# Performance work log

Hardware: AMD Instinct MI355X
Metric: run time of the kernel (lower is better)

Reference implementation:

```python
import jax, jax.numpy as jnp
import numpy as np

B, M, D = 8, 1024, 768          # batch, tokens, model dim
N, P = 32, 32                   # experts, slots per expert (N*P == M)
K = 8                           # mix_k (router top-k)
H = 2048                        # expert MLP hidden dim
EPS = 1e-12


def setup_inputs() -> dict:
    key = jax.random.key(0)
    ks = jax.random.split(key, 6)
    std_d = 1.0 / np.sqrt(D)
    std_h = 1.0 / np.sqrt(H)
    return {
        "x": jax.random.normal(ks[0], (B, M, D), jnp.float32),
        "cluster_assignments": jax.random.randint(ks[1], (B, M, K), 0, N),
        "phi": jax.random.normal(ks[2], (D, N, P), jnp.float32) * std_d,
        "scale": jnp.ones((1,), jnp.float32),
        "w1": jax.random.normal(ks[3], (N, D, H), jnp.float32) * std_d,
        "b1": jnp.zeros((N, H), jnp.float32),
        "w2": jax.random.normal(ks[4], (N, H, D), jnp.float32) * std_h,
        "b2": jnp.zeros((N, D), jnp.float32),
    }


def _seg_mean(vals, idx, num_segments):
    # index_reduce(..., 'mean', include_self=False): empty segments stay 0
    s = jax.ops.segment_sum(vals, idx, num_segments=num_segments)
    c = jax.ops.segment_sum(jnp.ones((vals.shape[0], 1), vals.dtype), idx,
                            num_segments=num_segments)
    return jnp.where(c > 0, s / jnp.maximum(c, 1.0), 0.0)


def _compute_acmoe(x_flat, top_assign):
    # MAD-based per-cluster, per-dim scaling (mad=True, mix_weights=False)
    mean_kd = _seg_mean(x_flat, top_assign, N)                 # [N, D]
    centered = jnp.abs(x_flat - mean_kd[top_assign])           # [B*M, D]
    w_mad = _seg_mean(centered, top_assign, N)                 # [N, D]
    W = 1.0 / (w_mad + 0.35)
    top_clamp = 5.0 * W.mean()
    W = jnp.minimum(W, top_clamp)
    W = W / W.mean()
    return W[top_assign]                                       # [B*M, D]


def reference(x, cluster_assignments, phi, scale, w1, b1, w2, b2):
    # normalize tokens (dim=2) and phi (dim=0), scale phi
    xn = x / jnp.maximum(jnp.linalg.norm(x, axis=-1, keepdims=True), EPS)
    phin = scale * phi / jnp.maximum(jnp.linalg.norm(phi, axis=0, keepdims=True), EPS)

    # ACMoE feature re-weighting (no-grad in original)
    top_assign = cluster_assignments.reshape(-1, K)[:, 0]       # [B*M]
    Mw = jax.lax.stop_gradient(_compute_acmoe(
        jax.lax.stop_gradient(xn.reshape(-1, D)), top_assign))
    xn = (xn.reshape(-1, D) * Mw).reshape(B, M, D)

    logits = jnp.einsum('bmd,dnp->bmnp', xn, phin)              # [B,M,N,P]
    aff = logits.reshape(B, M, N * P)
    mixing_weights, slot_assignments = jax.lax.top_k(aff, K)    # [B,M,K]
    new_clusters = slot_assignments // P

    disp = jax.nn.softmax(logits, axis=1)                       # over tokens m
    comb = jax.nn.softmax(aff, axis=-1).reshape(B, M, N, P)     # over (n,p)

    xs = jnp.einsum('bmd,bmnp->bnpd', xn, disp)                 # [B,N,P,D]
    # per-expert MLP, batched over expert axis n
    h = jnp.einsum('bnpd,ndh->bnph', xs, w1) + b1[None, :, None, :]
    h = jax.nn.gelu(h, approximate=False)
    ys = jnp.einsum('bnph,nhd->bnpd', h, w2) + b2[None, :, None, :]

    y = jnp.einsum('bnpd,bmnp->bmd', ys, comb)                  # [B,M,D]
    return y, mixing_weights, new_clusters
```

## Files before the change

### kernel.cpp

```cpp
#include <hip/hip_runtime.h>
#include <cmath>

#define NB    8
#define MTOK  1024
#define BMT   8192
#define DD    768
#define NEXP  32
#define PSLOT 32
#define NP    1024
#define KTOP  8
#define HH    2048

#define SLICES 128
#define TPS    64

typedef unsigned short ushort;
typedef __attribute__((ext_vector_type(8))) short short8v;
typedef __attribute__((ext_vector_type(4))) short short4v;
typedef __attribute__((ext_vector_type(4))) float f32x4;

__device__ __forceinline__ ushort bf16_rne(float x) {
    unsigned u = __float_as_uint(x);
    unsigned r = (u + 0x7FFFu + ((u >> 16) & 1u)) >> 16;
    return (ushort)r;
}
__device__ __forceinline__ float bf16_to_f(ushort h) {
    return __uint_as_float(((unsigned)h) << 16);
}
__device__ __forceinline__ void split2(float x, ushort& hi, ushort& lo) {
    hi = bf16_rne(x);
    lo = bf16_rne(x - bf16_to_f(hi));
}

__device__ __forceinline__ void gl_lds16(const ushort* g, ushort* l) {
    __builtin_amdgcn_global_load_lds(
        (const __attribute__((address_space(1))) void*)g,
        (__attribute__((address_space(3))) void*)l, 16, 0, 0);
}

__global__ __launch_bounds__(256) void norm_x(const float* __restrict__ x, float* __restrict__ xn) {
    int tok = blockIdx.x;
    int t = threadIdx.x;
    const float* p = x + (long)tok * DD;
    float v0 = p[t], v1 = p[t + 256], v2 = p[t + 512];
    float ss = v0 * v0 + v1 * v1 + v2 * v2;
#pragma unroll
    for (int o = 32; o; o >>= 1) ss += __shfl_xor(ss, o);
    __shared__ float sred[4];
    if ((t & 63) == 0) sred[t >> 6] = ss;
    __syncthreads();
    ss = sred[0] + sred[1] + sred[2] + sred[3];
    float inv = 1.0f / fmaxf(sqrtf(ss), 1e-12f);
    float* q = xn + (long)tok * DD;
    q[t] = v0 * inv; q[t + 256] = v1 * inv; q[t + 512] = v2 * inv;
}

__global__ __launch_bounds__(256) void norm_phi_T(const float* __restrict__ phi, const float* __restrict__ scale,
                                                  ushort* __restrict__ phT_hi, ushort* __restrict__ phT_lo) {
    int np = blockIdx.x;
    int t = threadIdx.x;
    float ss = 0.f;
    for (int d = t; d < DD; d += 256) {
        float v = phi[(long)d * NP + np];
        ss += v * v;
    }
#pragma unroll
    for (int o = 32; o; o >>= 1) ss += __shfl_xor(ss, o);
    __shared__ float sred[4];
    if ((t & 63) == 0) sred[t >> 6] = ss;
    __syncthreads();
    ss = sred[0] + sred[1] + sred[2] + sred[3];
    float sc = scale[0] / fmaxf(sqrtf(ss), 1e-12f);
    for (int d = t; d < DD; d += 256) {
        float v = phi[(long)d * NP + np] * sc;
        ushort h, l; split2(v, h, l);
        phT_hi[(long)np * DD + d] = h;
        phT_lo[(long)np * DD + d] = l;
    }
}

__global__ __launch_bounds__(256) void cluster_sum(const float* __restrict__ xn, const int* __restrict__ ca,
                                                   float* __restrict__ spart, float* __restrict__ cntpart) {
    __shared__ float s[NEXP][256];
    __shared__ float cnt[NEXP];
    int chunk = blockIdx.x, slice = blockIdx.y, t = threadIdx.x;
#pragma unroll
    for (int n = 0; n < NEXP; ++n) s[n][t] = 0.f;
    if (t < NEXP) cnt[t] = 0.f;
    __syncthreads();
    int tok0 = slice * TPS;
    for (int i = 0; i < TPS; ++i) {
        int tok = tok0 + i;
        int a = ca[tok * KTOP];
        float v = xn[(long)tok * DD + chunk * 256 + t];
        s[a][t] += v;
        if (chunk == 0 && t == 0) cnt[a] += 1.f;
    }
    __syncthreads();
    for (int n = 0; n < NEXP; ++n)
        spart[(long)slice * (NEXP * DD) + n * DD + chunk * 256 + t] = s[n][t];
    if (chunk == 0 && t < NEXP) cntpart[slice * NEXP + t] = cnt[t];
}

__global__ __launch_bounds__(256) void reduce_parts(const float* __restrict__ part, float* __restrict__ outv,
                                                    const float* __restrict__ cntpart, float* __restrict__ ccnt,
                                                    int doCnt) {
    int i = blockIdx.x * 256 + threadIdx.x;
    float s = 0.f;
#pragma unroll 8
    for (int sl = 0; sl < SLICES; ++sl) s += part[(long)sl * (NEXP * DD) + i];
    outv[i] = s;
    if (doCnt && i < NEXP) {
        float c = 0.f;
#pragma unroll 8
        for (int sl = 0; sl < SLICES; ++sl) c += cntpart[sl * NEXP + i];
        ccnt[i] = c;
    }
}

__global__ __launch_bounds__(256) void cluster_mad(const float* __restrict__ xn, const int* __restrict__ ca,
                                                   const float* __restrict__ csum, const float* __restrict__ ccnt,
                                                   float* __restrict__ mpart) {
    __shared__ float md[NEXP][256];
    __shared__ float mean[NEXP][256];
    int chunk = blockIdx.x, slice = blockIdx.y, t = threadIdx.x;
#pragma unroll
    for (int n = 0; n < NEXP; ++n) {
        float c = ccnt[n];
        mean[n][t] = (c > 0.f) ? csum[n * DD + chunk * 256 + t] / c : 0.f;
        md[n][t] = 0.f;
    }
    __syncthreads();
    int tok0 = slice * TPS;
    for (int i = 0; i < TPS; ++i) {
        int tok = tok0 + i;
        int a = ca[tok * KTOP];
        float v = xn[(long)tok * DD + chunk * 256 + t];
        md[a][t] += fabsf(v - mean[a][t]);
    }
    __syncthreads();
    for (int n = 0; n < NEXP; ++n)
        mpart[(long)slice * (NEXP * DD) + n * DD + chunk * 256 + t] = md[n][t];
}

__global__ __launch_bounds__(1024) void compute_W(const float* __restrict__ cmad, const float* __restrict__ ccnt,
                                                  float* __restrict__ W) {
    __shared__ float s[16];
    int t = threadIdx.x;
    auto block_sum = [&](float v) -> float {
#pragma unroll
        for (int o = 32; o; o >>= 1) v += __shfl_xor(v, o);
        if ((t & 63) == 0) s[t >> 6] = v;
        __syncthreads();
        float tot = 0.f;
#pragma unroll
        for (int i = 0; i < 16; ++i) tot += s[i];
        __syncthreads();
        return tot;
    };
    const int TOT = NEXP * DD;
    float p = 0.f;
    for (int i = t; i < TOT; i += 1024) {
        int n = i / DD;
        float c = ccnt[n];
        float wm = (c > 0.f) ? cmad[i] / c : 0.f;
        p += 1.f / (wm + 0.35f);
    }
    float mean1 = block_sum(p) / (float)TOT;
    float clamp = 5.f * mean1;
    p = 0.f;
    for (int i = t; i < TOT; i += 1024) {
        int n = i / DD;
        float c = ccnt[n];
        float wm = (c > 0.f) ? cmad[i] / c : 0.f;
        p += fminf(1.f / (wm + 0.35f), clamp);
    }
    float mean2 = block_sum(p) / (float)TOT;
    float inv2 = 1.f / mean2;
    for (int i = t; i < TOT; i += 1024) {
        int n = i / DD;
        float c = ccnt[n];
        float wm = (c > 0.f) ? cmad[i] / c : 0.f;
        W[i] = fminf(1.f / (wm + 0.35f), clamp) * inv2;
    }
}

__global__ __launch_bounds__(192) void apply_W(float* __restrict__ xn, const int* __restrict__ ca,
                                               const float* __restrict__ W,
                                               ushort* __restrict__ hi, ushort* __restrict__ lo) {
    int tok = blockIdx.x;
    long d4 = (long)tok * DD + threadIdx.x * 4;
    int a = ca[tok * KTOP];
    float4 v = *reinterpret_cast<float4*>(xn + d4);
    float4 w = *reinterpret_cast<const float4*>(W + a * DD + threadIdx.x * 4);
    v.x *= w.x; v.y *= w.y; v.z *= w.z; v.w *= w.w;
    *reinterpret_cast<float4*>(xn + d4) = v;
    ushort h0,h1,h2,h3,l0,l1,l2,l3;
    split2(v.x,h0,l0); split2(v.y,h1,l1); split2(v.z,h2,l2); split2(v.w,h3,l3);
    *reinterpret_cast<short4v*>(hi + d4) = short4v{(short)h0,(short)h1,(short)h2,(short)h3};
    *reinterpret_cast<short4v*>(lo + d4) = short4v{(short)l0,(short)l1,(short)l2,(short)l3};
}

template <bool PAIR, int AMAP, int EPI, bool CBF16, int CMAP>
__global__ __launch_bounds__(256) void gemm2(
    const ushort* __restrict__ Ah_g, const ushort* __restrict__ Al_g,
    const float*  __restrict__ Bf_g,
    const ushort* __restrict__ Bh_g, const ushort* __restrict__ Bl_g,
    float* __restrict__ Cf, ushort* __restrict__ Cb,
    int K, int lda, int ldb, int ldc,
    long sA, long sB, long sC,
    const float* __restrict__ bias, int biasStride) {
    constexpr int BUFS = PAIR ? 12288 : 8192;
    constexpr int BM   = PAIR ? 64 : 128;
    constexpr int MI   = PAIR ? 2 : 4;
    __shared__ __attribute__((aligned(16))) ushort lds[3 * BUFS];

    int orig = blockIdx.x + gridDim.x * (blockIdx.y + gridDim.y * blockIdx.z);
    int nwg = gridDim.x * gridDim.y * gridDim.z;
    int wg = (orig & 7) * (nwg >> 3) + (orig >> 3);
    int bx = wg % gridDim.x;
    int rest = wg / gridDim.x;
    int by = rest % gridDim.y;
    int z  = rest / gridDim.y;
    const int m0 = by * BM;
    const int n0 = bx * 128;

    const int tid = threadIdx.x, lane = tid & 63, w = tid >> 6;
    const int wr = w >> 1, wc = w & 1;
    const int lr = lane & 15, kh = lane >> 4;

    const int NCA = PAIR ? 1 : 2;
    long arowA[2]; int kOffA[2];
#pragma unroll
    for (int i = 0; i < NCA; ++i) {
        int c = i * 256 + tid;
        int r = c >> 2, sp = c & 3;
        kOffA[i] = (sp ^ ((r >> 1) & 3)) << 3;
        int rg = m0 + r;
        if constexpr (AMAP == 0) arowA[i] = (long)z * sA + (long)rg * lda;
        else arowA[i] = ((long)(rg >> 5) * 1024 + (long)z * 32 + (rg & 31)) * (long)lda;
    }
    long browB[2]; int kOffB[2];
#pragma unroll
    for (int i = 0; i < 2; ++i) {
        int c = i * 256 + tid;
        int r = c >> 2, sp = c & 3;
        kOffB[i] = (sp ^ ((r >> 1) & 3)) << 3;
        browB[i] = (long)(n0 + r) * ldb;
    }
    const int kq = tid & 7, nq = tid >> 3;

    f32x4 acc[MI][4];
#pragma unroll
    for (int i = 0; i < MI; ++i)
#pragma unroll
        for (int j = 0; j < 4; ++j) acc[i][j] = (f32x4)(0.f);

    auto stageA = [&](int buf, int kk0) {
        const int bb = buf * BUFS;
        if constexpr (PAIR) {
            gl_lds16(Ah_g + arowA[0] + kk0 + kOffA[0], &lds[bb + (w * 64) * 8]);
            gl_lds16(Al_g + arowA[0] + kk0 + kOffA[0], &lds[bb + 2048 + (w * 64) * 8]);
#pragma unroll
            for (int i = 0; i < 2; ++i) {
                int base = bb + 4096 + (i * 256 + w * 64) * 8;
                gl_lds16(Bh_g + browB[i] + kk0 + kOffB[i], &lds[base]);
                gl_lds16(Bl_g + browB[i] + kk0 + kOffB[i], &lds[base + 4096]);
            }
        } else {
#pragma unroll
            for (int i = 0; i < 2; ++i)
                gl_lds16(Ah_g + arowA[i] + kk0 + kOffA[i], &lds[bb + (i * 256 + w * 64) * 8]);
        }
    };

    auto loadB = [&](float4 (&rB)[4], int kk0) {
#pragma unroll
        for (int dk = 0; dk < 4; ++dk)
            rB[dk] = *reinterpret_cast<const float4*>(
                Bf_g + (long)z * sB + (long)(kk0 + kq * 4 + dk) * ldb + n0 + nq * 4);
    };

    auto bwrite = [&](int buf, float4 (&rB)[4]) {
        ushort hv[4][4];
#pragma unroll
        for (int dk = 0; dk < 4; ++dk) {
            hv[dk][0] = bf16_rne(rB[dk].x); hv[dk][1] = bf16_rne(rB[dk].y);
            hv[dk][2] = bf16_rne(rB[dk].z); hv[dk][3] = bf16_rne(rB[dk].w);
        }
#pragma unroll
        for (int dn = 0; dn < 4; ++dn) {
            int n = nq * 4 + dn;
            int phys = (kq >> 1) ^ ((n >> 1) & 3);
            int off = buf * BUFS + 4096 + n * 32 + phys * 8 + (kq & 1) * 4;
            *reinterpret_cast<short4v*>(&lds[off]) =
                short4v{(short)hv[0][dn], (short)hv[1][dn], (short)hv[2][dn], (short)hv[3][dn]};
        }
    };

    auto compute = [&](int buf) {
        const int aB = buf * BUFS;
        const int bB = buf * BUFS + 4096;
        short8v bh[4], bl[4];
#pragma unroll
        for (int nj = 0; nj < 4; ++nj) {
            int rb = wc * 64 + nj * 16 + lr;
            int off = bB + rb * 32 + ((kh ^ ((rb >> 1) & 3)) << 3);
            bh[nj] = *reinterpret_cast<const short8v*>(&lds[off]);
            if constexpr (PAIR) bl[nj] = *reinterpret_cast<const short8v*>(&lds[off + 4096]);
        }
#pragma unroll
        for (int mi = 0; mi < MI; ++mi) {
            int ra = wr * (PAIR ? 32 : 64) + mi * 16 + lr;
            int off = aB + ra * 32 + ((kh ^ ((ra >> 1) & 3)) << 3);
            short8v ah = *reinterpret_cast<const short8v*>(&lds[off]);
            if constexpr (PAIR) {
                short8v al = *reinterpret_cast<const short8v*>(&lds[off + 2048]);
#pragma unroll
                for (int nj = 0; nj < 4; ++nj) {
                    acc[mi][nj] = __builtin_amdgcn_mfma_f32_16x16x32_bf16(ah, bh[nj], acc[mi][nj], 0, 0, 0);
                    acc[mi][nj] = __builtin_amdgcn_mfma_f32_16x16x32_bf16(ah, bl[nj], acc[mi][nj], 0, 0, 0);
                    acc[mi][nj] = __builtin_amdgcn_mfma_f32_16x16x32_bf16(al, bh[nj], acc[mi][nj], 0, 0, 0);
                }
            } else {
#pragma unroll
                for (int nj = 0; nj < 4; ++nj)
                    acc[mi][nj] = __builtin_amdgcn_mfma_f32_16x16x32_bf16(ah, bh[nj], acc[mi][nj], 0, 0, 0);
            }
        }
    };

    const int nt = K >> 5;
    if constexpr (PAIR) {
        stageA(0, 0);
        stageA(1, 32);
        asm volatile("s_waitcnt vmcnt(6)" ::: "memory");
        __builtin_amdgcn_s_barrier();
        __builtin_amdgcn_sched_barrier(0);
        int cc = 0, cn2 = 2;
        for (int t = 0; t < nt; ++t) {
            bool deep = (t + 2 < nt);
            if (deep) stageA(cn2, (t + 2) << 5);
            compute(cc);
            if (deep) { asm volatile("s_waitcnt vmcnt(6)" ::: "memory"); }
            else      { asm volatile("s_waitcnt vmcnt(0)" ::: "memory"); }
            if (t + 1 < nt) {
                __builtin_amdgcn_s_barrier();
                __builtin_amdgcn_sched_barrier(0);
            }
            cc = (cc == 2) ? 0 : cc + 1;
            cn2 = (cn2 == 2) ? 0 : cn2 + 1;
        }
    } else {
        float4 rBa[4], rBb[4];
        loadB(rBa, 0);
        bwrite(0, rBa);
        stageA(0, 0);
        stageA(1, 32);
        loadB(rBb, 32);
        asm volatile("s_waitcnt vmcnt(6) lgkmcnt(0)" ::: "memory");
        __builtin_amdgcn_s_barrier();
        __builtin_amdgcn_sched_barrier(0);
        int cc = 0, cn1 = 1, cn2 = 2;
        auto iter = [&](int t, float4 (&ld)[4], float4 (&wr_)[4]) {
            bool deep = (t + 2 < nt);
            if (deep) { stageA(cn2, (t + 2) << 5); loadB(ld, (t + 2) << 5); }
            compute(cc);
            if (t + 1 < nt) bwrite(cn1, wr_);
            if (deep) { asm volatile("s_waitcnt vmcnt(6) lgkmcnt(0)" ::: "memory"); }
            else      { asm volatile("s_waitcnt vmcnt(0) lgkmcnt(0)" ::: "memory"); }
            if (t + 1 < nt) {
                __builtin_amdgcn_s_barrier();
                __builtin_amdgcn_sched_barrier(0);
            }
            cc = (cc == 2) ? 0 : cc + 1;
            cn1 = (cn1 == 2) ? 0 : cn1 + 1;
            cn2 = (cn2 == 2) ? 0 : cn2 + 1;
        };
        for (int t = 0; t < nt; t += 2) {
            iter(t, rBa, rBb);
            iter(t + 1, rBb, rBa);
        }
    }

#pragma unroll
    for (int mi = 0; mi < MI; ++mi)
#pragma unroll
        for (int j = 0; j < 4; ++j) {
            int rg = m0 + wr * (PAIR ? 32 : 64) + mi * 16 + kh * 4 + j;
            long roff;
            if constexpr (CMAP == 1) roff = ((long)(rg >> 5) * 1024 + (long)z * 32 + (rg & 31)) * (long)ldc;
            else                     roff = (long)z * sC + (long)rg * ldc;
#pragma unroll
            for (int nj = 0; nj < 4; ++nj) {
                int col = n0 + wc * 64 + nj * 16 + lr;
                float v = acc[mi][nj][j];
                if constexpr (EPI >= 1) v += bias[(long)z * biasStride + col];
                if constexpr (EPI == 2) v = 0.5f * v * (1.0f + erff(v * 0.70710678118654752f));
                if constexpr (CBF16) Cb[roff + col] = bf16_rne(v);
                else                 Cf[roff + col] = v;
            }
        }
}

__global__ __launch_bounds__(64) void row_topk(const float* __restrict__ logits,
                                               float* __restrict__ mix_out, float* __restrict__ clus_out,
                                               float* __restrict__ rowmax, float* __restrict__ rowsumInv) {
    int row = blockIdx.x;
    int lane = threadIdx.x;
    const float* p = logits + (long)row * NP;
    float v[16];
#pragma unroll
    for (int i = 0; i < 16; ++i) v[i] = p[lane + i * 64];
    float mx = v[0];
#pragma unroll
    for (int i = 1; i < 16; ++i) mx = fmaxf(mx, v[i]);
#pragma unroll
    for (int o = 32; o; o >>= 1) mx = fmaxf(mx, __shfl_xor(mx, o));
    float s = 0.f;
#pragma unroll
    for (int i = 0; i < 16; ++i) s += __expf(v[i] - mx);
#pragma unroll
    for (int o = 32; o; o >>= 1) s += __shfl_xor(s, o);
    if (lane == 0) { rowmax[row] = mx; rowsumInv[row] = 1.0f / s; }
#pragma unroll
    for (int k = 0; k < KTOP; ++k) {
        float bv = -INFINITY; int bi = 1 << 30;
#pragma unroll
        for (int i = 0; i < 16; ++i) {
            if (v[i] > bv) { bv = v[i]; bi = lane + i * 64; }
        }
#pragma unroll
        for (int o = 32; o; o >>= 1) {
            float ov = __shfl_xor(bv, o); int oi = __shfl_xor(bi, o);
            if (ov > bv || (ov == bv && oi < bi)) { bv = ov; bi = oi; }
        }
        int owner = bi & 63, slot = bi >> 6;
        if (lane == owner) {
#pragma unroll
            for (int i = 0; i < 16; ++i) if (slot == i) v[i] = -INFINITY;
        }
        if (lane == k) {
            mix_out[(long)row * KTOP + k] = bv;
            clus_out[(long)row * KTOP + k] = (float)(bi >> 5);
        }
    }
}

__global__ __launch_bounds__(256) void col_stats_part(const float* __restrict__ logits,
                                                      float* __restrict__ pmax, float* __restrict__ psum) {
    int b = blockIdx.z, ms = blockIdx.y, npc = blockIdx.x;
    int np = npc * 256 + threadIdx.x;
    const float* p = logits + ((long)b * MTOK + ms * 128) * NP + np;
    float mx = -INFINITY, s = 0.f;
    for (int m = 0; m < 128; ++m) {
        float v = p[(long)m * NP];
        float nm = fmaxf(mx, v);
        s = s * __expf(mx - nm) + __expf(v - nm);
        mx = nm;
    }
    long o = ((long)b * 8 + ms) * NP + np;
    pmax[o] = mx; psum[o] = s;
}

__global__ __launch_bounds__(256) void col_stats_merge(const float* __restrict__ pmax, const float* __restrict__ psum,
                                                       float* __restrict__ cmax, float* __restrict__ csumInv) {
    int b = blockIdx.y;
    int np = blockIdx.x * 256 + threadIdx.x;
    float mx = -INFINITY;
#pragma unroll
    for (int ms = 0; ms < 8; ++ms) mx = fmaxf(mx, pmax[((long)b * 8 + ms) * NP + np]);
    float s = 0.f;
#pragma unroll
    for (int ms = 0; ms < 8; ++ms) {
        long o = ((long)b * 8 + ms) * NP + np;
        s += psum[o] * __expf(pmax[o] - mx);
    }
    cmax[(long)b * NP + np] = mx;
    csumInv[(long)b * NP + np] = 1.0f / s;
}

__global__ __launch_bounds__(256) void make_dispT(const float* __restrict__ logits,
                                                  const float* __restrict__ cmax, const float* __restrict__ cinv,
                                                  ushort* __restrict__ dispT) {
    __shared__ float tile[64][65];
    int b = blockIdx.z, np0 = blockIdx.x * 64, m0 = blockIdx.y * 64;
    int tr = threadIdx.x >> 6, tc = threadIdx.x & 63;
    const float* src = logits + ((long)b * MTOK + m0) * NP + np0;
#pragma unroll
    for (int i = 0; i < 16; ++i) {
        int m = tr * 16 + i;
        tile[m][tc] = src[(long)m * NP + tc];
    }
    __syncthreads();
#pragma unroll
    for (int i = 0; i < 16; ++i) {
        int npl = tr * 16 + i;
        int np = np0 + npl;
        float mx = cmax[(long)b * NP + np], iv = cinv[(long)b * NP + np];
        float v = __expf(tile[tc][npl] - mx) * iv;
        dispT[((long)b * NP + np) * MTOK + (m0 + tc)] = bf16_rne(v);
    }
}

__global__ __launch_bounds__(256) void make_comb(const float* __restrict__ logits,
                                                 const float* __restrict__ rmax, const float* __restrict__ rinv,
                                                 ushort* __restrict__ comb) {
    long base = ((long)blockIdx.x * 256 + threadIdx.x) * 4;
    int row = (int)(base >> 10);
    float mx = rmax[row], iv = rinv[row];
    float4 v = *reinterpret_cast<const float4*>(logits + base);
    *reinterpret_cast<short4v*>(comb + base) = short4v{
        (short)bf16_rne(__expf(v.x - mx) * iv), (short)bf16_rne(__expf(v.y - mx) * iv),
        (short)bf16_rne(__expf(v.z - mx) * iv), (short)bf16_rne(__expf(v.w - mx) * iv)};
}

extern "C" void kernel_launch(void* const* d_in, const int* in_sizes, int n_in,
                              void* d_out, int out_size, void* d_ws, size_t ws_size,
                              hipStream_t stream) {
    const float* x    = (const float*)d_in[0];
    const int*   ca   = (const int*)d_in[1];
    const float* phi  = (const float*)d_in[2];
    const float* scale= (const float*)d_in[3];
    const float* w1   = (const float*)d_in[4];
    const float* b1   = (const float*)d_in[5];
    const float* w2   = (const float*)d_in[6];
    const float* b2   = (const float*)d_in[7];
    float* out = (float*)d_out;
    float* ws  = (float*)d_ws;

    float*  xn       = ws;
    float*  logits   = xn + 6291456;
    ushort* xnp_hi   = (ushort*)(logits + 8388608);
    ushort* xnp_lo   = xnp_hi + 6291456;
    ushort* phT_hi   = xnp_lo + 6291456;
    ushort* phT_lo   = phT_hi + 786432;
    ushort* dispT_bf = phT_lo + 786432;
    ushort* comb_bf  = dispT_bf + 8388608;
    ushort* xs_bf    = comb_bf + 8388608;
    ushort* h_bf     = xs_bf + 6291456;
    float*  stats    = (float*)(h_bf + 16777216);
    float* rowmax    = stats;
    float* rowsumInv = rowmax + 8192;
    float* colmax    = rowsumInv + 8192;
    float* colsumInv = colmax + 8192;
    float* pmax      = colsumInv + 8192;
    float* psum      = pmax + 65536;
    float* csum      = psum + 65536;
    float* cmad      = csum + 24576;
    float* Wbuf      = cmad + 24576;
    float* ccnt      = Wbuf + 24576;
    float* cntpart   = ccnt + 64;
    float* spart     = cntpart + 4096;
    float* mpart     = spart + 3145728;
    float* ys        = xn;

    float* out_y    = out;
    float* out_mix  = out + 6291456;
    float* out_clus = out + 6291456 + 65536;

    norm_x<<<BMT, 256, 0, stream>>>(x, xn);
    norm_phi_T<<<NP, 256, 0, stream>>>(phi, scale, phT_hi, phT_lo);

    cluster_sum<<<dim3(3, SLICES), 256, 0, stream>>>(xn, ca, spart, cntpart);
    reduce_parts<<<96, 256, 0, stream>>>(spart, csum, cntpart, ccnt, 1);
    cluster_mad<<<dim3(3, SLICES), 256, 0, stream>>>(xn, ca, csum, ccnt, mpart);
    reduce_parts<<<96, 256, 0, stream>>>(mpart, cmad, nullptr, nullptr, 0);
    compute_W<<<1, 1024, 0, stream>>>(cmad, ccnt, Wbuf);
    apply_W<<<BMT, 192, 0, stream>>>(xn, ca, Wbuf, xnp_hi, xnp_lo);

    gemm2<true, 0, 0, false, 0><<<dim3(8, 128, 1), 256, 0, stream>>>(
        xnp_hi, xnp_lo, nullptr, phT_hi, phT_lo, logits, nullptr,
        DD, DD, DD, NP, 0, 0, 0, nullptr, 0);

    row_topk<<<BMT, 64, 0, stream>>>(logits, out_mix, out_clus, rowmax, rowsumInv);
    col_stats_part<<<dim3(4, 8, NB), 256, 0, stream>>>(logits, pmax, psum);
    col_stats_merge<<<dim3(4, NB), 256, 0, stream>>>(pmax, psum, colmax, colsumInv);
    make_dispT<<<dim3(16, 16, NB), 256, 0, stream>>>(logits, colmax, colsumInv, dispT_bf);
    make_comb<<<8192, 256, 0, stream>>>(logits, rowmax, rowsumInv, comb_bf);

    gemm2<false, 0, 0, true, 0><<<dim3(6, 8, NB), 256, 0, stream>>>(
        dispT_bf, nullptr, xn, nullptr, nullptr, nullptr, xs_bf,
        MTOK, MTOK, DD, DD,
        (long)NP * MTOK, (long)MTOK * DD, (long)NP * DD, nullptr, 0);

    gemm2<false, 1, 2, true, 0><<<dim3(16, 2, NEXP), 256, 0, stream>>>(
        xs_bf, nullptr, w1, nullptr, nullptr, nullptr, h_bf,
        DD, DD, HH, HH,
        0, (long)DD * HH, (long)256 * HH, b1, HH);

    gemm2<false, 0, 1, false, 1><<<dim3(6, 2, NEXP), 256, 0, stream>>>(
        h_bf, nullptr, w2, nullptr, nullptr, ys, nullptr,
        HH, HH, DD, DD,
        (long)256 * HH, (long)HH * DD, 0, b2, DD);

    gemm2<false, 0, 0, false, 0><<<dim3(6, 8, NB), 256, 0, stream>>>(
        comb_bf, nullptr, ys, nullptr, nullptr, out_y, nullptr,
        NP, NP, DD, DD,
        (long)MTOK * NP, (long)NP * DD, (long)MTOK * DD, nullptr, 0);
}
```

Baseline: 515.7 us.

## Pre-transpose B operands to bf16 and stage them via direct global-to-LDS loads

Adds a tiled transpose kernel that writes the xn high part and the expert outputs ys as transposed bf16 matrices. The dispatch and combine GEMMs then run in a new mode that loads both A and B into LDS with async direct loads, instead of reading fp32 B into registers and converting it. This is meant to cut B-side global traffic and conversion work inside the GEMM loop, at the cost of two extra transpose passes and more workspace. It also changes B for the dispatch GEMM from the fp32 xn to only the bf16 high part, which slightly alters precision.

Result: faster. 490.0 us (-5.0%).

```diff
diff --git a/kernel.cpp b/kernel.cpp
--- a/kernel.cpp
+++ b/kernel.cpp
@@ -201,7 +201,41 @@
     *reinterpret_cast<short4v*>(lo + d4) = short4v{(short)l0,(short)l1,(short)l2,(short)l3};
 }
 
-template <bool PAIR, int AMAP, int EPI, bool CBF16, int CMAP>
+template <bool F32>
+__global__ __launch_bounds__(256) void make_T(const void* __restrict__ srcv, ushort* __restrict__ dst,
+                                              int R, int C) {
+    __shared__ ushort tile[64][65];
+    int z = blockIdx.z;
+    int c0 = blockIdx.x * 64, r0 = blockIdx.y * 64;
+    int tr = threadIdx.x >> 4;
+    int tc4 = (threadIdx.x & 15) * 4;
+    long base = (long)z * R * C;
+#pragma unroll
+    for (int i = 0; i < 4; ++i) {
+        int r = tr + i * 16;
+        if constexpr (F32) {
+            const float* s = (const float*)srcv;
+            float4 v = *reinterpret_cast<const float4*>(s + base + (long)(r0 + r) * C + c0 + tc4);
+            tile[r][tc4 + 0] = bf16_rne(v.x); tile[r][tc4 + 1] = bf16_rne(v.y);
+            tile[r][tc4 + 2] = bf16_rne(v.z); tile[r][tc4 + 3] = bf16_rne(v.w);
+        } else {
+            const ushort* s = (const ushort*)srcv;
+            short4v v = *reinterpret_cast<const short4v*>(s + base + (long)(r0 + r) * C + c0 + tc4);
+            tile[r][tc4 + 0] = (ushort)v.x; tile[r][tc4 + 1] = (ushort)v.y;
+            tile[r][tc4 + 2] = (ushort)v.z; tile[r][tc4 + 3] = (ushort)v.w;
+        }
+    }
+    __syncthreads();
+#pragma unroll
+    for (int i = 0; i < 4; ++i) {
+        int oc = tr + i * 16;
+        short4v o = short4v{(short)tile[tc4 + 0][oc], (short)tile[tc4 + 1][oc],
+                            (short)tile[tc4 + 2][oc], (short)tile[tc4 + 3][oc]};
+        *reinterpret_cast<short4v*>(dst + base + (long)(c0 + oc) * R + r0 + tc4) = o;
+    }
+}
+
+template <int MODE, int AMAP, int EPI, bool CBF16, int CMAP>
 __global__ __launch_bounds__(256) void gemm2(
     const ushort* __restrict__ Ah_g, const ushort* __restrict__ Al_g,
     const float*  __restrict__ Bf_g,
@@ -210,6 +244,7 @@
     int K, int lda, int ldb, int ldc,
     long sA, long sB, long sC,
     const float* __restrict__ bias, int biasStride) {
+    constexpr bool PAIR = (MODE == 1);
     constexpr int BUFS = PAIR ? 12288 : 8192;
     constexpr int BM   = PAIR ? 64 : 128;
     constexpr int MI   = PAIR ? 2 : 4;
@@ -246,7 +281,7 @@
         int c = i * 256 + tid;
         int r = c >> 2, sp = c & 3;
         kOffB[i] = (sp ^ ((r >> 1) & 3)) << 3;
-        browB[i] = (long)(n0 + r) * ldb;
+        browB[i] = (long)z * sB + (long)(n0 + r) * ldb;
     }
     const int kq = tid & 7, nq = tid >> 3;
 
@@ -258,7 +293,7 @@
 
     auto stageA = [&](int buf, int kk0) {
         const int bb = buf * BUFS;
-        if constexpr (PAIR) {
+        if constexpr (MODE == 1) {
             gl_lds16(Ah_g + arowA[0] + kk0 + kOffA[0], &lds[bb + (w * 64) * 8]);
             gl_lds16(Al_g + arowA[0] + kk0 + kOffA[0], &lds[bb + 2048 + (w * 64) * 8]);
 #pragma unroll
@@ -267,6 +302,13 @@
                 gl_lds16(Bh_g + browB[i] + kk0 + kOffB[i], &lds[base]);
                 gl_lds16(Bl_g + browB[i] + kk0 + kOffB[i], &lds[base + 4096]);
             }
+        } else if constexpr (MODE == 0) {
+#pragma unroll
+            for (int i = 0; i < 2; ++i)
+                gl_lds16(Ah_g + arowA[i] + kk0 + kOffA[i], &lds[bb + (i * 256 + w * 64) * 8]);
+#pragma unroll
+            for (int i = 0; i < 2; ++i)
+                gl_lds16(Bh_g + browB[i] + kk0 + kOffB[i], &lds[bb + 4096 + (i * 256 + w * 64) * 8]);
         } else {
 #pragma unroll
             for (int i = 0; i < 2; ++i)
@@ -331,10 +373,11 @@
     };
 
     const int nt = K >> 5;
-    if constexpr (PAIR) {
+    if constexpr (MODE == 0 || MODE == 1) {
         stageA(0, 0);
         stageA(1, 32);
-        asm volatile("s_waitcnt vmcnt(6)" ::: "memory");
+        if constexpr (MODE == 1) { asm volatile("s_waitcnt vmcnt(6)" ::: "memory"); }
+        else                     { asm volatile("s_waitcnt vmcnt(4)" ::: "memory"); }
         __builtin_amdgcn_s_barrier();
         __builtin_amdgcn_sched_barrier(0);
         int cc = 0, cn2 = 2;
@@ -342,8 +385,12 @@
             bool deep = (t + 2 < nt);
             if (deep) stageA(cn2, (t + 2) << 5);
             compute(cc);
-            if (deep) { asm volatile("s_waitcnt vmcnt(6)" ::: "memory"); }
-            else      { asm volatile("s_waitcnt vmcnt(0)" ::: "memory"); }
+            if (deep) {
+                if constexpr (MODE == 1) { asm volatile("s_waitcnt vmcnt(6)" ::: "memory"); }
+                else                     { asm volatile("s_waitcnt vmcnt(4)" ::: "memory"); }
+            } else {
+                asm volatile("s_waitcnt vmcnt(0)" ::: "memory");
+            }
             if (t + 1 < nt) {
                 __builtin_amdgcn_s_barrier();
                 __builtin_amdgcn_sched_barrier(0);
@@ -539,7 +586,9 @@
     ushort* comb_bf  = dispT_bf + 8388608;
     ushort* xs_bf    = comb_bf + 8388608;
     ushort* h_bf     = xs_bf + 6291456;
-    float*  stats    = (float*)(h_bf + 16777216);
+    ushort* xnT_bf   = h_bf + 16777216;
+    ushort* ysT_bf   = xnT_bf + 6291456;
+    float*  stats    = (float*)(ysT_bf + 6291456);
     float* rowmax    = stats;
     float* rowsumInv = rowmax + 8192;
     float* colmax    = rowsumInv + 8192;
@@ -569,7 +618,9 @@
     compute_W<<<1, 1024, 0, stream>>>(cmad, ccnt, Wbuf);
     apply_W<<<BMT, 192, 0, stream>>>(xn, ca, Wbuf, xnp_hi, xnp_lo);
 
-    gemm2<true, 0, 0, false, 0><<<dim3(8, 128, 1), 256, 0, stream>>>(
+    make_T<false><<<dim3(12, 16, NB), 256, 0, stream>>>(xnp_hi, xnT_bf, MTOK, DD);
+
+    gemm2<1, 0, 0, false, 0><<<dim3(8, 128, 1), 256, 0, stream>>>(
         xnp_hi, xnp_lo, nullptr, phT_hi, phT_lo, logits, nullptr,
         DD, DD, DD, NP, 0, 0, 0, nullptr, 0);
 
@@ -579,23 +630,25 @@
     make_dispT<<<dim3(16, 16, NB), 256, 0, stream>>>(logits, colmax, colsumInv, dispT_bf);
     make_comb<<<8192, 256, 0, stream>>>(logits, rowmax, rowsumInv, comb_bf);
 
-    gemm2<false, 0, 0, true, 0><<<dim3(6, 8, NB), 256, 0, stream>>>(
-        dispT_bf, nullptr, xn, nullptr, nullptr, nullptr, xs_bf,
-        MTOK, MTOK, DD, DD,
-        (long)NP * MTOK, (long)MTOK * DD, (long)NP * DD, nullptr, 0);
-
-    gemm2<false, 1, 2, true, 0><<<dim3(16, 2, NEXP), 256, 0, stream>>>(
+    gemm2<0, 0, 0, true, 0><<<dim3(6, 8, NB), 256, 0, stream>>>(
+        dispT_bf, nullptr, nullptr, xnT_bf, nullptr, nullptr, xs_bf,
+        MTOK, MTOK, MTOK, DD,
+        (long)NP * MTOK, (long)DD * MTOK, (long)NP * DD, nullptr, 0);
+
+    gemm2<2, 1, 2, true, 0><<<dim3(16, 2, NEXP), 256, 0, stream>>>(
         xs_bf, nullptr, w1, nullptr, nullptr, nullptr, h_bf,
         DD, DD, HH, HH,
         0, (long)DD * HH, (long)256 * HH, b1, HH);
 
-    gemm2<false, 0, 1, false, 1><<<dim3(6, 2, NEXP), 256, 0, stream>>>(
+    gemm2<2, 0, 1, false, 1><<<dim3(6, 2, NEXP), 256, 0, stream>>>(
         h_bf, nullptr, w2, nullptr, nullptr, ys, nullptr,
         HH, HH, DD, DD,
         (long)256 * HH, (long)HH * DD, 0, b2, DD);
 
-    gemm2<false, 0, 0, false, 0><<<dim3(6, 8, NB), 256, 0, stream>>>(
-        comb_bf, nullptr, ys, nullptr, nullptr, out_y, nullptr,
-        NP, NP, DD, DD,
-        (long)MTOK * NP, (long)NP * DD, (long)MTOK * DD, nullptr, 0);
-}
+    make_T<true><<<dim3(12, 16, NB), 256, 0, stream>>>(ys, ysT_bf, MTOK, DD);
+
+    gemm2<0, 0, 0, false, 0><<<dim3(6, 8, NB), 256, 0, stream>>>(
+        comb_bf, nullptr, nullptr, ysT_bf, nullptr, out_y, nullptr,
+        NP, NP, NP, DD,
+        (long)MTOK * NP, (long)DD * NP, (long)MTOK * DD, nullptr, 0);
+}
```
